# Optimization experiments

Measured on AMD Instinct MI355X. Metric: run time of the kernel, lower is better.

The kernel has to match this reference:

```python
import jax, jax.numpy as jnp
import numpy as np

J = 58        # n_joints (two 29-joint dancers)
NIN = 192     # n_in
H = 512       # n_hid
NOUT = 128    # n_out
B = 32        # batch


def _xavier(key, fan_in, fan_out):
    return jax.random.normal(key, (fan_in, fan_out), jnp.float32) * jnp.sqrt(2.0 / (fan_in + fan_out))


def setup_inputs() -> dict:
    key = jax.random.key(0)
    ks = jax.random.split(key, 8)
    # fully-connected directed graph, no self loops: E = J*(J-1) = 3306
    src_np, dst_np = np.nonzero(1 - np.eye(J, dtype=np.int32))
    edge_index = jnp.asarray(np.stack([src_np, dst_np]), dtype=jnp.int32)  # [2, E]
    x = jax.random.normal(ks[0], (B, 1, J, NIN), jnp.float32)
    return dict(
        x=x,
        edge_index=edge_index,
        gcn1_w=_xavier(ks[1], NIN, H), gcn1_b=jnp.full((H,), 0.1, jnp.float32),
        mlp1_w=_xavier(ks[2], 2 * H, H), mlp1_b=jnp.full((H,), 0.1, jnp.float32),
        bn1_g=jnp.ones((H,), jnp.float32), bn1_b=jnp.zeros((H,), jnp.float32),
        gcn2_w=_xavier(ks[3], H, H), gcn2_b=jnp.full((H,), 0.1, jnp.float32),
        mlp2_w=_xavier(ks[4], 3 * H, H), mlp2_b=jnp.full((H,), 0.1, jnp.float32),
        bn2_g=jnp.ones((H,), jnp.float32), bn2_b=jnp.zeros((H,), jnp.float32),
        fc_w=_xavier(ks[5], H, NOUT), fc_b=jnp.full((NOUT,), 0.1, jnp.float32),
    )


def _gcn_norm_adj(edge_index, n_nodes, dtype):
    # PyG GCNConv default: A_hat = A + I, sym-normalized D^-1/2 A_hat D^-1/2
    src, dst = edge_index[0], edge_index[1]
    adj = jnp.zeros((n_nodes, n_nodes), dtype).at[dst, src].add(1.0) + jnp.eye(n_nodes, dtype=dtype)
    d_inv_sqrt = 1.0 / jnp.sqrt(adj.sum(axis=1))
    return d_inv_sqrt[:, None] * adj * d_inv_sqrt[None, :]


def _batchnorm(h, gamma, beta):
    # BatchNorm1d (training-mode stats) over (batch, length) per channel
    mu = h.mean(axis=(0, 1))
    var = h.var(axis=(0, 1))
    return (h - mu) * jax.lax.rsqrt(var + 1e-5) * gamma + beta


def reference(x, edge_index, gcn1_w, gcn1_b, mlp1_w, mlp1_b, bn1_g, bn1_b,
              gcn2_w, gcn2_b, mlp2_w, mlp2_b, bn2_g, bn2_b, fc_w, fc_b):
    b = x.shape[0]
    n = x.shape[2]
    x = x.reshape(b, n, -1)                                  # [B, J, n_in]
    src, dst = edge_index[0], edge_index[1]
    A = _gcn_norm_adj(edge_index, n, x.dtype)                # [J, J]

    # GCNConv 1 + relu
    h = jax.nn.relu(jnp.einsum('ij,bjf->bif', A, x) @ gcn1_w + gcn1_b)   # [B, J, H]
    # node2edge: concat(sender, receiver) feats -> MLP1 -> BN (batched gather)
    e = jnp.concatenate([h[:, src], h[:, dst]], axis=-1)     # [B, E, 2H]
    e = jax.nn.relu(e @ mlp1_w + mlp1_b)                     # [B, E, H]
    e = _batchnorm(e, bn1_g, bn1_b)                          # dropout p=0 -> identity
    x_skip = e
    # edge2node: sum incoming edge feats per receiver node (m_in^T @ e)
    node = jnp.zeros((b, n, e.shape[-1]), e.dtype).at[:, dst].add(e)     # [B, J, H]

    # GCNConv 2 + relu
    h2 = jax.nn.relu(jnp.einsum('ij,bjf->bif', A, node) @ gcn2_w + gcn2_b)
    # node2edge again, concat skip, MLP2, BN, fc_out
    e2 = jnp.concatenate([h2[:, src], h2[:, dst], x_skip], axis=-1)      # [B, E, 3H]
    e2 = jax.nn.relu(e2 @ mlp2_w + mlp2_b)
    e2 = _batchnorm(e2, bn2_g, bn2_b)
    return e2 @ fc_w + fc_b                                  # [B, E, n_out]
```

## Files before the change

kernel.cpp:

```cpp
#include <hip/hip_runtime.h>
#include <stdint.h>

#define J_ 58
#define E_ 3306
#define B_ 32
#define NIN_ 192
#define H_ 512
#define NOUT_ 128
#define M_EDGE (B_*E_)
#define M_PAD  (M_EDGE + 64)
#define M_NODE (B_*J_)
#define NSLOT 64

typedef unsigned short u16;
typedef __attribute__((ext_vector_type(8))) short short8v;
typedef __attribute__((ext_vector_type(4))) float f32x4;

__device__ __forceinline__ float b2f(u16 u){ return __uint_as_float(((uint32_t)u)<<16); }
__device__ __forceinline__ u16 f2b(float f){
  uint32_t u = __float_as_uint(f);
  u += 0x7FFFu + ((u>>16)&1u);
  return (u16)(u>>16);
}
__device__ __forceinline__ void async16(const void* g, void* l){
  __builtin_amdgcn_global_load_lds((const __attribute__((address_space(1))) uint32_t*)g,
                                   (__attribute__((address_space(3))) uint32_t*)l, 16, 0, 0);
}

__global__ __launch_bounds__(256) void build_graph(const int* __restrict__ ei,
    float* __restrict__ Adj, float* __restrict__ aind,
    int* __restrict__ csroff, int* __restrict__ csredg)
{
  __shared__ float adj[J_][J_];
  __shared__ int   deg[J_];
  __shared__ float dinv[J_];
  __shared__ int   off[J_+1];
  __shared__ int   cur[J_];
  const int t = threadIdx.x;
  const int* srcI = ei;
  const int* dstI = ei + E_;
  for (int i = t; i < J_*J_; i += 256) adj[i/J_][i%J_] = 0.f;
  if (t < J_) { deg[t] = 0; cur[t] = 0; }
  __syncthreads();
  for (int e = t; e < E_; e += 256) {
    atomicAdd(&adj[dstI[e]][srcI[e]], 1.f);
    atomicAdd(&deg[dstI[e]], 1);
  }
  __syncthreads();
  if (t < J_) adj[t][t] += 1.f;
  __syncthreads();
  if (t < J_) {
    float s = 0.f;
    for (int j = 0; j < J_; ++j) s += adj[t][j];
    dinv[t] = rsqrtf(s);
  }
  __syncthreads();
  for (int i = t; i < J_*J_; i += 256) {
    int r = i / J_, c = i % J_;
    Adj[i] = dinv[r]*adj[r][c]*dinv[c];
  }
  if (t < J_) {
    float s = 0.f;
    for (int j = 0; j < J_; ++j) s += dinv[t]*adj[t][j]*dinv[j]*(float)deg[j];
    aind[t] = s;
  }
  if (t == 0) {
    off[0] = 0;
    for (int n = 0; n < J_; ++n) off[n+1] = off[n] + deg[n];
  }
  __syncthreads();
  if (t <= J_) csroff[t] = off[t];
  for (int e = t; e < E_; e += 256) {
    int d = dstI[e];
    int p = atomicAdd(&cur[d], 1);
    csredg[off[d] + p] = e;
  }
}

__global__ __launch_bounds__(256) void transpose_cv(const float* __restrict__ src,
    u16* __restrict__ dst, int K, int N)
{
  int idx = blockIdx.x*256 + threadIdx.x;
  if (idx >= K*N) return;
  int k = idx / N, n = idx - k*N;
  dst[(size_t)n*K + k] = f2b(src[idx]);
}

__global__ __launch_bounds__(192) void ax_kernel(const float* __restrict__ Adj,
    const float* __restrict__ x, u16* __restrict__ Ax)
{
  int bi = blockIdx.x;
  int b = bi / J_, i = bi - b*J_;
  __shared__ float Arow[J_];
  if (threadIdx.x < J_) Arow[threadIdx.x] = Adj[i*J_ + threadIdx.x];
  __syncthreads();
  int f = threadIdx.x;
  const float* xb = x + (size_t)b*J_*NIN_ + f;
  float acc = 0.f;
  for (int j = 0; j < J_; ++j) acc += Arow[j]*xb[(size_t)j*NIN_];
  Ax[(size_t)bi*NIN_ + f] = f2b(acc);
}

template<int MODE>
__global__ __launch_bounds__(256) void gemm64(
    const u16* __restrict__ Aop, const u16* __restrict__ Bt,
    const int M, const int N, const int K,
    const float* __restrict__ bias,
    u16* __restrict__ outB, float* __restrict__ outF)
{
  __shared__ __align__(16) u16 Al[64*32];
  __shared__ __align__(16) u16 Bl[64*32];
  const int tid = threadIdx.x;
  const int w = tid >> 6, l = tid & 63;
  const int row0 = blockIdx.x * 64, col0 = blockIdx.y * 64;
  f32x4 acc[4] = {};
  const u16* ag = Aop + (size_t)(row0 + (tid>>2))*K + (tid&3)*8;
  const u16* bg = Bt  + (size_t)(col0 + (tid>>2))*K + (tid&3)*8;
  const int fr = l & 15, fg = l >> 4;
  const int nk = K >> 5;
  for (int kt = 0; kt < nk; ++kt) {
    short8v av = *(const short8v*)ag;
    short8v bv = *(const short8v*)bg;
    ag += 32; bg += 32;
    __syncthreads();
    *(short8v*)(Al + tid*8) = av;
    *(short8v*)(Bl + tid*8) = bv;
    __syncthreads();
    short8v a = *(const short8v*)(Al + (w*16 + fr)*32 + fg*8);
#pragma unroll
    for (int nt = 0; nt < 4; ++nt) {
      short8v b = *(const short8v*)(Bl + (nt*16 + fr)*32 + fg*8);
      acc[nt] = __builtin_amdgcn_mfma_f32_16x16x32_bf16(a, b, acc[nt], 0, 0, 0);
    }
  }
#pragma unroll
  for (int nt = 0; nt < 4; ++nt) {
    int gc = col0 + nt*16 + fr;
    float bv = (MODE == 1) ? bias[gc] : 0.f;
#pragma unroll
    for (int r = 0; r < 4; ++r) {
      int gr = row0 + w*16 + fg*4 + r;
      if (MODE == 0) outF[(size_t)gr*N + gc] = acc[nt][r];
      else           outB[(size_t)gr*N + gc] = f2b(fmaxf(acc[nt][r] + bv, 0.f));
    }
  }
}

template<int MODE>
__global__ __launch_bounds__(256) void gemm128(
    const u16* __restrict__ Aop, const u16* __restrict__ Bt,
    const int N, const int K,
    const float* __restrict__ g1, const float* __restrict__ g2,
    const float* __restrict__ crow,
    const int* __restrict__ srcI, const int* __restrict__ dstI,
    double* __restrict__ sumslot, double* __restrict__ sqslot,
    u16* __restrict__ outB, float* __restrict__ outF)
{
  __shared__ __align__(16) u16 Al[128*32];
  __shared__ __align__(16) u16 Bl[128*32];
  const int tid = threadIdx.x;
  const int w = tid >> 6, l = tid & 63;
  const int wm = w >> 1, wn = w & 1;
  const int row0 = blockIdx.x * 128, col0 = blockIdx.y * 128;
  const int fr = l & 15, fg = l >> 4;
  f32x4 acc[4][4] = {};
  const int srow = l >> 2, skoff = (l & 3) * 8;
  const u16* agA = Aop + (size_t)(row0 + w*16 + srow)*K + skoff;
  const u16* agB = Bt  + (size_t)(col0 + w*16 + srow)*K + skoff;
  const size_t rstep = (size_t)64 * K;
  u16* ldsA0 = Al + w*512;
  u16* ldsA1 = Al + 2048 + w*512;
  u16* ldsB0 = Bl + w*512;
  u16* ldsB1 = Bl + 2048 + w*512;
  const int nk = K >> 5;
  for (int kt = 0; kt < nk; ++kt) {
    __syncthreads();
    async16(agA,         ldsA0);
    async16(agA + rstep, ldsA1);
    async16(agB,         ldsB0);
    async16(agB + rstep, ldsB1);
    agA += 32; agB += 32;
    __syncthreads();
    short8v a[4], b[4];
#pragma unroll
    for (int i = 0; i < 4; ++i)
      a[i] = *(const short8v*)(Al + (wm*64 + i*16 + fr)*32 + fg*8);
#pragma unroll
    for (int j = 0; j < 4; ++j)
      b[j] = *(const short8v*)(Bl + (wn*64 + j*16 + fr)*32 + fg*8);
#pragma unroll
    for (int i = 0; i < 4; ++i)
#pragma unroll
      for (int j = 0; j < 4; ++j)
        acc[i][j] = __builtin_amdgcn_mfma_f32_16x16x32_bf16(a[i], b[j], acc[i][j], 0, 0, 0);
  }

  if (MODE == 2) {
    int mr[4][4];
    uint32_t off1[4][4], off2[4][4];
#pragma unroll
    for (int i = 0; i < 4; ++i)
#pragma unroll
      for (int r = 0; r < 4; ++r) {
        int m = row0 + wm*64 + i*16 + fg*4 + r;
        mr[i][r] = m;
        int mm = (m < M_EDGE) ? m : 0;
        uint32_t bb = (uint32_t)mm / E_;
        uint32_t ke = (uint32_t)mm - bb*E_;
        off1[i][r] = (bb*J_ + (uint32_t)srcI[ke])*H_;
        off2[i][r] = (bb*J_ + (uint32_t)dstI[ke])*H_;
      }
    const int slot = blockIdx.x & (NSLOT-1);
#pragma unroll
    for (int j = 0; j < 4; ++j) {
      int gc = col0 + wn*64 + j*16 + fr;
      float cr = crow[gc];
      double s = 0.0, q = 0.0;
#pragma unroll
      for (int i = 0; i < 4; ++i)
#pragma unroll
        for (int r = 0; r < 4; ++r) {
          float v = acc[i][j][r] + g1[off1[i][r] + gc] + g2[off2[i][r] + gc] + cr;
          v = fmaxf(v, 0.f);
          if (mr[i][r] < M_EDGE) {
            outB[(size_t)mr[i][r]*N + gc] = f2b(v);
            double vd = (double)v;
            s += vd; q += vd*vd;
          }
        }
      s += __shfl_xor(s, 16); s += __shfl_xor(s, 32);
      q += __shfl_xor(q, 16); q += __shfl_xor(q, 32);
      if (fg == 0) {
        atomicAdd(&sumslot[(size_t)slot*H_ + gc], s);
        atomicAdd(&sqslot [(size_t)slot*H_ + gc], q);
      }
    }
  } else {
#pragma unroll
    for (int j = 0; j < 4; ++j) {
      int gc = col0 + wn*64 + j*16 + fr;
      float cr = crow[gc];
#pragma unroll
      for (int i = 0; i < 4; ++i)
#pragma unroll
        for (int r = 0; r < 4; ++r) {
          int m = row0 + wm*64 + i*16 + fg*4 + r;
          if (m < M_EDGE) outF[(size_t)m*N + gc] = acc[i][j][r] + cr;
        }
    }
  }
}

__global__ __launch_bounds__(256) void edge1_kernel(const float* __restrict__ hs,
    const float* __restrict__ hd, const float* __restrict__ b1,
    const int* __restrict__ srcI, const int* __restrict__ dstI,
    u16* __restrict__ e_raw, double* __restrict__ sumslot, double* __restrict__ sqslot)
{
  const int t = threadIdx.x;
  const int row0 = blockIdx.x * 16;
  float bv0 = b1[t], bv1 = b1[t+256];
  double s0=0.0,q0=0.0,s1=0.0,q1=0.0;
  for (int r = 0; r < 16; ++r) {
    int m = row0 + r;
    uint32_t bb = (uint32_t)m / E_;
    uint32_t ke = (uint32_t)m - bb*E_;
    const float* ps = hs + ((size_t)bb*J_ + srcI[ke])*H_;
    const float* pd = hd + ((size_t)bb*J_ + dstI[ke])*H_;
    float v0 = fmaxf(ps[t]     + pd[t]     + bv0, 0.f);
    float v1 = fmaxf(ps[t+256] + pd[t+256] + bv1, 0.f);
    e_raw[(size_t)m*H_ + t]       = f2b(v0);
    e_raw[(size_t)m*H_ + t + 256] = f2b(v1);
    double d0 = (double)v0, d1 = (double)v1;
    s0 += d0; q0 += d0*d0; s1 += d1; q1 += d1*d1;
  }
  const int slot = blockIdx.x & (NSLOT-1);
  atomicAdd(&sumslot[(size_t)slot*H_ + t],     s0);
  atomicAdd(&sumslot[(size_t)slot*H_ + t+256], s1);
  atomicAdd(&sqslot [(size_t)slot*H_ + t],     q0);
  atomicAdd(&sqslot [(size_t)slot*H_ + t+256], q1);
}

__global__ __launch_bounds__(512) void bn_fin(const double* __restrict__ sumslot,
    const double* __restrict__ sqslot, const float* __restrict__ g, const float* __restrict__ b,
    float* __restrict__ scale, float* __restrict__ shift)
{
  int c = threadIdx.x;
  double s = 0.0, q = 0.0;
  for (int k = 0; k < NSLOT; ++k) { s += sumslot[(size_t)k*H_ + c]; q += sqslot[(size_t)k*H_ + c]; }
  const double invM = 1.0 / (double)M_EDGE;
  double mu = s * invM;
  double var = q * invM - mu*mu;
  if (var < 0.0) var = 0.0;
  float sc = g[c] * (float)(1.0 / sqrt(var + 1e-5));
  scale[c] = sc;
  shift[c] = b[c] - (float)mu*sc;
}

__global__ __launch_bounds__(256) void build_wc(const float* __restrict__ m2w,
    const float* __restrict__ m2b, const float* __restrict__ scale1, const float* __restrict__ shift1,
    u16* __restrict__ WcT, float* __restrict__ crow)
{
  int n = blockIdx.x;
  int t = threadIdx.x;
  __shared__ float red[256];
  float part = 0.f;
  for (int k = t; k < H_; k += 256) {
    float wv = m2w[(size_t)(2*H_ + k)*H_ + n];
    WcT[(size_t)n*H_ + k] = f2b(scale1[k]*wv);
    part += shift1[k]*wv;
  }
  red[t] = part; __syncthreads();
  for (int s = 128; s; s >>= 1) { if (t < s) red[t] += red[t+s]; __syncthreads(); }
  if (t == 0) crow[n] = red[0] + m2b[n];
}

__global__ __launch_bounds__(256) void build_fc(const float* __restrict__ fcw,
    const float* __restrict__ fcb, const float* __restrict__ scale2, const float* __restrict__ shift2,
    u16* __restrict__ fcT, float* __restrict__ cvec)
{
  int n = blockIdx.x;
  int t = threadIdx.x;
  __shared__ float red[256];
  float part = 0.f;
  for (int k = t; k < H_; k += 256) {
    float wv = fcw[(size_t)k*NOUT_ + n];
    fcT[(size_t)n*H_ + k] = f2b(scale2[k]*wv);
    part += shift2[k]*wv;
  }
  red[t] = part; __syncthreads();
  for (int s = 128; s; s >>= 1) { if (t < s) red[t] += red[t+s]; __syncthreads(); }
  if (t == 0) cvec[n] = red[0] + fcb[n];
}

__global__ __launch_bounds__(256) void scatter_kernel(const u16* __restrict__ e_raw,
    const int* __restrict__ csroff, const int* __restrict__ csredg, float* __restrict__ node_raw)
{
  int bi = blockIdx.x;
  int b = bi / J_, n = bi - b*J_;
  int beg = csroff[n], end = csroff[n+1];
  int c0 = threadIdx.x, c1 = threadIdx.x + 256;
  float a0 = 0.f, a1 = 0.f;
  for (int p = beg; p < end; ++p) {
    const u16* er = e_raw + ((size_t)b*E_ + csredg[p])*H_;
    a0 += b2f(er[c0]); a1 += b2f(er[c1]);
  }
  node_raw[(size_t)bi*H_ + c0] = a0;
  node_raw[(size_t)bi*H_ + c1] = a1;
}

__global__ __launch_bounds__(256) void an_kernel(const float* __restrict__ Adj,
    const float* __restrict__ node_raw, const float* __restrict__ scale1,
    const float* __restrict__ shift1, const float* __restrict__ aind, u16* __restrict__ An)
{
  int bi = blockIdx.x;
  int b = bi / J_, i = bi - b*J_;
  __shared__ float Arow[J_];
  if (threadIdx.x < J_) Arow[threadIdx.x] = Adj[i*J_ + threadIdx.x];
  __syncthreads();
  float ai = aind[i];
#pragma unroll
  for (int h = 0; h < 2; ++h) {
    int c = threadIdx.x + h*256;
    const float* nb = node_raw + (size_t)b*J_*H_ + c;
    float acc = 0.f;
    for (int j = 0; j < J_; ++j) acc += Arow[j]*nb[(size_t)j*H_];
    An[(size_t)bi*H_ + c] = f2b(scale1[c]*acc + shift1[c]*ai);
  }
}

extern "C" void kernel_launch(void* const* d_in, const int* in_sizes, int n_in,
                              void* d_out, int out_size, void* d_ws, size_t ws_size,
                              hipStream_t stream)
{
  const float* x    = (const float*)d_in[0];
  const int*   ei   = (const int*)d_in[1];
  const float* g1w  = (const float*)d_in[2];
  const float* g1b  = (const float*)d_in[3];
  const float* m1w  = (const float*)d_in[4];
  const float* m1b  = (const float*)d_in[5];
  const float* bn1g = (const float*)d_in[6];
  const float* bn1b = (const float*)d_in[7];
  const float* g2w  = (const float*)d_in[8];
  const float* g2b  = (const float*)d_in[9];
  const float* m2w  = (const float*)d_in[10];
  const float* m2b  = (const float*)d_in[11];
  const float* bn2g = (const float*)d_in[12];
  const float* bn2b = (const float*)d_in[13];
  const float* fcw  = (const float*)d_in[14];
  const float* fcb  = (const float*)d_in[15];

  char* wsp = (char*)d_ws;
  size_t off = 0;
  auto alloc = [&](size_t bytes) -> char* {
    char* p = wsp + off;
    off = (off + bytes + 255) & ~(size_t)255;
    return p;
  };
  float* Adj    = (float*)alloc(J_*J_*4);
  float* aind   = (float*)alloc(J_*4);
  int*   csroff = (int*)alloc((J_+1)*4);
  int*   csredg = (int*)alloc(E_*4);
  float* scale1 = (float*)alloc(H_*4);
  float* shift1 = (float*)alloc(H_*4);
  float* scale2 = (float*)alloc(H_*4);
  float* shift2 = (float*)alloc(H_*4);
  float* crow1  = (float*)alloc(H_*4);
  float* cvec   = (float*)alloc(NOUT_*4);
  double* slots = (double*)alloc((size_t)4*NSLOT*H_*8);
  double* sum1 = slots;
  double* sq1  = slots + (size_t)NSLOT*H_;
  double* sum2 = slots + (size_t)2*NSLOT*H_;
  double* sq2  = slots + (size_t)3*NSLOT*H_;
  u16* g1T  = (u16*)alloc((size_t)H_*NIN_*2);
  u16* g2T  = (u16*)alloc((size_t)H_*H_*2);
  u16* W1aT = (u16*)alloc((size_t)H_*H_*2);
  u16* W1bT = (u16*)alloc((size_t)H_*H_*2);
  u16* W2aT = (u16*)alloc((size_t)H_*H_*2);
  u16* W2bT = (u16*)alloc((size_t)H_*H_*2);
  u16* WcT  = (u16*)alloc((size_t)H_*H_*2);
  u16* fcT  = (u16*)alloc((size_t)NOUT_*H_*2);
  u16* Ax   = (u16*)alloc((size_t)M_NODE*NIN_*2);
  u16* h    = (u16*)alloc((size_t)M_NODE*H_*2);
  float* hs = (float*)alloc((size_t)M_NODE*H_*4);
  float* hd = (float*)alloc((size_t)M_NODE*H_*4);
  float* node_raw = (float*)alloc((size_t)M_NODE*H_*4);
  u16* An   = (u16*)alloc((size_t)M_NODE*H_*2);
  u16* h2   = (u16*)alloc((size_t)M_NODE*H_*2);
  float* h2s = (float*)alloc((size_t)M_NODE*H_*4);
  float* h2d = (float*)alloc((size_t)M_NODE*H_*4);
  u16* e_raw = (u16*)alloc((size_t)M_PAD*H_*2);
  u16* e2    = (u16*)alloc((size_t)M_PAD*H_*2);
  if (off > ws_size) return;

  const int* srcI = ei;
  const int* dstI = ei + E_;
  float* outF = (float*)d_out;

  hipMemsetAsync(slots, 0, (size_t)4*NSLOT*H_*8, stream);
  build_graph<<<1, 256, 0, stream>>>(ei, Adj, aind, csroff, csredg);

  transpose_cv<<<(NIN_*H_+255)/256, 256, 0, stream>>>(g1w, g1T, NIN_, H_);
  transpose_cv<<<(H_*H_+255)/256, 256, 0, stream>>>(g2w, g2T, H_, H_);
  transpose_cv<<<(H_*H_+255)/256, 256, 0, stream>>>(m1w, W1aT, H_, H_);
  transpose_cv<<<(H_*H_+255)/256, 256, 0, stream>>>(m1w + (size_t)H_*H_, W1bT, H_, H_);
  transpose_cv<<<(H_*H_+255)/256, 256, 0, stream>>>(m2w, W2aT, H_, H_);
  transpose_cv<<<(H_*H_+255)/256, 256, 0, stream>>>(m2w + (size_t)H_*H_, W2bT, H_, H_);

  ax_kernel<<<M_NODE, 192, 0, stream>>>(Adj, x, Ax);

  gemm64<1><<<dim3(M_NODE/64, H_/64), 256, 0, stream>>>(Ax, g1T, M_NODE, H_, NIN_,
      g1b, h, nullptr);
  gemm64<0><<<dim3(M_NODE/64, H_/64), 256, 0, stream>>>(h, W1aT, M_NODE, H_, H_,
      nullptr, nullptr, hs);
  gemm64<0><<<dim3(M_NODE/64, H_/64), 256, 0, stream>>>(h, W1bT, M_NODE, H_, H_,
      nullptr, nullptr, hd);
  edge1_kernel<<<M_EDGE/16, 256, 0, stream>>>(hs, hd, m1b, srcI, dstI, e_raw, sum1, sq1);
  bn_fin<<<1, 512, 0, stream>>>(sum1, sq1, bn1g, bn1b, scale1, shift1);
  build_wc<<<H_, 256, 0, stream>>>(m2w, m2b, scale1, shift1, WcT, crow1);
  scatter_kernel<<<M_NODE, 256, 0, stream>>>(e_raw, csroff, csredg, node_raw);
  an_kernel<<<M_NODE, 256, 0, stream>>>(Adj, node_raw, scale1, shift1, aind, An);
  gemm64<1><<<dim3(M_NODE/64, H_/64), 256, 0, stream>>>(An, g2T, M_NODE, H_, H_,
      g2b, h2, nullptr);
  gemm64<0><<<dim3(M_NODE/64, H_/64), 256, 0, stream>>>(h2, W2aT, M_NODE, H_, H_,
      nullptr, nullptr, h2s);
  gemm64<0><<<dim3(M_NODE/64, H_/64), 256, 0, stream>>>(h2, W2bT, M_NODE, H_, H_,
      nullptr, nullptr, h2d);
  gemm128<2><<<dim3(M_PAD/128, H_/128), 256, 0, stream>>>(e_raw, WcT, H_, H_,
      h2s, h2d, crow1, srcI, dstI, sum2, sq2, e2, nullptr);
  bn_fin<<<1, 512, 0, stream>>>(sum2, sq2, bn2g, bn2b, scale2, shift2);
  build_fc<<<NOUT_, 256, 0, stream>>>(fcw, fcb, scale2, shift2, fcT, cvec);
  gemm128<3><<<dim3(M_PAD/128, NOUT_/128), 256, 0, stream>>>(e2, fcT, NOUT_, H_,
      nullptr, nullptr, cvec, nullptr, nullptr, nullptr, nullptr, nullptr, outF);
}
```

Baseline: 557.5 us.

## Double-buffer LDS tiles in gemm128 to overlap global loads with MFMA

The shared-memory A/B tiles in gemm128 become ping-pong buffers. The next K-slice is issued asynchronously before the MFMA work on the current slice, so each iteration needs one barrier instead of two. The launch bounds also now ask for at least 3 blocks per CU. The larger LDS footprint (32 KB per block) and the occupancy hint could limit registers or residency, and the overlap only happens if the async copies do not wait internally.

Measured after the change: 500.1 us. 1.11x faster.

```diff
diff --git a/kernel.cpp b/kernel.cpp
--- a/kernel.cpp
+++ b/kernel.cpp
@@ -147,7 +147,7 @@
 }
 
 template<int MODE>
-__global__ __launch_bounds__(256) void gemm128(
+__global__ __launch_bounds__(256, 3) void gemm128(
     const u16* __restrict__ Aop, const u16* __restrict__ Bt,
     const int N, const int K,
     const float* __restrict__ g1, const float* __restrict__ g2,
@@ -156,8 +156,8 @@
     double* __restrict__ sumslot, double* __restrict__ sqslot,
     u16* __restrict__ outB, float* __restrict__ outF)
 {
-  __shared__ __align__(16) u16 Al[128*32];
-  __shared__ __align__(16) u16 Bl[128*32];
+  __shared__ __align__(16) u16 Al[2][128*32];
+  __shared__ __align__(16) u16 Bl[2][128*32];
   const int tid = threadIdx.x;
   const int w = tid >> 6, l = tid & 63;
   const int wm = w >> 1, wn = w & 1;
@@ -168,31 +168,35 @@
   const u16* agA = Aop + (size_t)(row0 + w*16 + srow)*K + skoff;
   const u16* agB = Bt  + (size_t)(col0 + w*16 + srow)*K + skoff;
   const size_t rstep = (size_t)64 * K;
-  u16* ldsA0 = Al + w*512;
-  u16* ldsA1 = Al + 2048 + w*512;
-  u16* ldsB0 = Bl + w*512;
-  u16* ldsB1 = Bl + 2048 + w*512;
   const int nk = K >> 5;
+  async16(agA,         &Al[0][w*512]);
+  async16(agA + rstep, &Al[0][2048 + w*512]);
+  async16(agB,         &Bl[0][w*512]);
+  async16(agB + rstep, &Bl[0][2048 + w*512]);
+  __syncthreads();
   for (int kt = 0; kt < nk; ++kt) {
-    __syncthreads();
-    async16(agA,         ldsA0);
-    async16(agA + rstep, ldsA1);
-    async16(agB,         ldsB0);
-    async16(agB + rstep, ldsB1);
-    agA += 32; agB += 32;
-    __syncthreads();
+    const int cur = kt & 1, nxt = cur ^ 1;
+    if (kt + 1 < nk) {
+      const u16* pa = agA + (kt+1)*32;
+      const u16* pb = agB + (kt+1)*32;
+      async16(pa,         &Al[nxt][w*512]);
+      async16(pa + rstep, &Al[nxt][2048 + w*512]);
+      async16(pb,         &Bl[nxt][w*512]);
+      async16(pb + rstep, &Bl[nxt][2048 + w*512]);
+    }
     short8v a[4], b[4];
 #pragma unroll
     for (int i = 0; i < 4; ++i)
-      a[i] = *(const short8v*)(Al + (wm*64 + i*16 + fr)*32 + fg*8);
+      a[i] = *(const short8v*)(&Al[cur][(wm*64 + i*16 + fr)*32 + fg*8]);
 #pragma unroll
     for (int j = 0; j < 4; ++j)
-      b[j] = *(const short8v*)(Bl + (wn*64 + j*16 + fr)*32 + fg*8);
+      b[j] = *(const short8v*)(&Bl[cur][(wn*64 + j*16 + fr)*32 + fg*8]);
 #pragma unroll
     for (int i = 0; i < 4; ++i)
 #pragma unroll
       for (int j = 0; j < 4; ++j)
         acc[i][j] = __builtin_amdgcn_mfma_f32_16x16x32_bf16(a[i], b[j], acc[i][j], 0, 0, 0);
+    __syncthreads();
   }
 
   if (MODE == 2) {
```
